# Performance work log

Measured on AMD Instinct MI355X. Metric: run time of the kernel, lower is better.

The kernel has to match this reference:

```python
import jax, jax.numpy as jnp
import numpy as np

H = 2048      # hidden_size
NH = 16       # num attention heads
KVH = 4       # num kv heads (GQA)
D = 128       # head_dim
E = 32        # num experts
K = 4         # top-k experts per token
I = 768       # moe intermediate size
T = 1024      # num tokens (single prefill sequence)
EPS = 1e-6
THETA = 10000.0


def rmsnorm(x, w, eps=EPS):
    return x * jax.lax.rsqrt(jnp.mean(x * x, axis=-1, keepdims=True) + eps) * w


def rope_cos_sin(positions, dim, theta):
    inv_freq = 1.0 / (theta ** (jnp.arange(0, dim, 2, dtype=jnp.float32) / dim))
    freqs = positions.astype(jnp.float32)[:, None] * inv_freq[None, :]   # [T, D/2]
    emb = jnp.concatenate([freqs, freqs], axis=-1)                       # [T, D]
    return jnp.cos(emb), jnp.sin(emb)


def apply_rope(x, cos, sin):
    # x: [T, nH, D]; cos/sin: [T, D] -> neox style: cat(-x2, x1)
    x1, x2 = jnp.split(x, 2, axis=-1)
    x_rot = jnp.concatenate([-x2, x1], axis=-1)
    return cos[:, None, :] * x + sin[:, None, :] * x_rot


def setup_inputs() -> dict:
    key = jax.random.key(0)
    ks = jax.random.split(key, 8)
    s = 0.02
    return {
        "hidden_states": jax.random.normal(ks[0], (T, H), jnp.float32),
        "positions": jnp.arange(T, dtype=jnp.int32),
        "ln1_w": jnp.ones((H,), jnp.float32),
        "w_qkv": jax.random.normal(ks[1], ((NH + 2 * KVH) * D, H), jnp.float32) * s,
        "q_norm_w": jnp.ones((D,), jnp.float32),
        "k_norm_w": jnp.ones((D,), jnp.float32),
        "w_o": jax.random.normal(ks[2], (H, NH * D), jnp.float32) * s,
        "ln2_w": jnp.ones((H,), jnp.float32),
        "router_w": jax.random.normal(ks[3], (E, H), jnp.float32) * s,
        "w_gate": jax.random.normal(ks[4], (E, I, H), jnp.float32) * s,
        "w_up": jax.random.normal(ks[5], (E, I, H), jnp.float32) * s,
        "w_down": jax.random.normal(ks[6], (E, H, I), jnp.float32) * s,
    }


def decoder_layer(hidden_states, positions, ln1_w, w_qkv, q_norm_w, k_norm_w,
                  w_o, ln2_w, router_w, w_gate, w_up, w_down):
    # ---- attention block ----
    residual = hidden_states
    h = rmsnorm(hidden_states, ln1_w)

    qkv = h @ w_qkv.T                                      # [T, (NH+2*KVH)*D]
    q, k, v = jnp.split(qkv, [NH * D, (NH + KVH) * D], axis=-1)
    q = q.reshape(T, NH, D)
    k = k.reshape(T, KVH, D)
    v = v.reshape(T, KVH, D)

    # per-head RMSNorm on q and k (Qwen3 QK-norm)
    q = rmsnorm(q, q_norm_w)
    k = rmsnorm(k, k_norm_w)

    cos, sin = rope_cos_sin(positions, D, THETA)
    q = apply_rope(q, cos, sin)
    k = apply_rope(k, cos, sin)

    rep = NH // KVH
    k = jnp.repeat(k, rep, axis=1)                         # [T, NH, D]
    v = jnp.repeat(v, rep, axis=1)

    scale = D ** -0.5
    scores = jnp.einsum("qhd,khd->hqk", q, k) * scale      # [NH, T, T]
    causal = jnp.tril(jnp.ones((T, T), bool))
    scores = jnp.where(causal[None], scores, -1e30)
    probs = jax.nn.softmax(scores, axis=-1)
    attn = jnp.einsum("hqk,khd->qhd", probs, v).reshape(T, NH * D)
    attn_out = attn @ w_o.T                                # [T, H]

    hidden = residual + attn_out

    # ---- MoE block ----
    residual = hidden
    h = rmsnorm(hidden, ln2_w)

    logits = h @ router_w.T                                # [T, E]
    router_probs = jax.nn.softmax(logits, axis=-1)
    topk_w, topk_idx = jax.lax.top_k(router_probs, K)      # softmax-then-topk
    topk_w = topk_w / (jnp.sum(topk_w, axis=-1, keepdims=True) + 1e-20)

    # scatter top-k weights into a dense [T, E] combine matrix
    combine = jnp.zeros((T, E), h.dtype).at[
        jnp.arange(T)[:, None], topk_idx].add(topk_w)

    gate = jnp.einsum("th,eih->tei", h, w_gate)            # [T, E, I]
    up = jnp.einsum("th,eih->tei", h, w_up)
    act = jax.nn.silu(gate) * up
    moe_out = jnp.einsum("tei,ehi,te->th", act, w_down, combine)

    return residual + moe_out


def reference(hidden_states, positions, ln1_w, w_qkv, q_norm_w, k_norm_w,
              w_o, ln2_w, router_w, w_gate, w_up, w_down):
    return decoder_layer(hidden_states, positions, ln1_w, w_qkv, q_norm_w,
                         k_norm_w, w_o, ln2_w, router_w, w_gate, w_up, w_down)
```

## Files before the change

### kernel.cpp

```cpp
#include <hip/hip_runtime.h>

typedef __attribute__((ext_vector_type(4))) float f32x4;
typedef __attribute__((ext_vector_type(8))) __bf16 bf16x8;
typedef __attribute__((ext_vector_type(4))) __bf16 bf16x4;

__device__ __forceinline__ f32x4 mfma16(bf16x8 a, bf16x8 b, f32x4 c) {
  return __builtin_amdgcn_mfma_f32_16x16x32_bf16(a, b, c, 0, 0, 0);
}

__global__ __launch_bounds__(256) void rmsnorm_k(const float* __restrict__ x,
                                                 const float* __restrict__ w,
                                                 float* __restrict__ y,
                                                 __bf16* __restrict__ yb) {
  int t = blockIdx.x;
  const float* xr = x + (size_t)t * 2048;
  int d0 = threadIdx.x * 4;
  float4 v1 = *(const float4*)(xr + d0);
  float4 v2 = *(const float4*)(xr + 1024 + d0);
  float ss = v1.x*v1.x + v1.y*v1.y + v1.z*v1.z + v1.w*v1.w
           + v2.x*v2.x + v2.y*v2.y + v2.z*v2.z + v2.w*v2.w;
#pragma unroll
  for (int mk = 1; mk < 64; mk <<= 1) ss += __shfl_xor(ss, mk);
  __shared__ float red[4];
  if ((threadIdx.x & 63) == 0) red[threadIdx.x >> 6] = ss;
  __syncthreads();
  float tot = red[0] + red[1] + red[2] + red[3];
  float rs = rsqrtf(tot * (1.0f / 2048.0f) + 1e-6f);
  float* yr = y + (size_t)t * 2048;
  float4 w1 = *(const float4*)(w + d0);
  float4 w2 = *(const float4*)(w + 1024 + d0);
  float4 o1, o2;
  o1.x = v1.x*rs*w1.x; o1.y = v1.y*rs*w1.y; o1.z = v1.z*rs*w1.z; o1.w = v1.w*rs*w1.w;
  o2.x = v2.x*rs*w2.x; o2.y = v2.y*rs*w2.y; o2.z = v2.z*rs*w2.z; o2.w = v2.w*rs*w2.w;
  *(float4*)(yr + d0) = o1;
  *(float4*)(yr + 1024 + d0) = o2;
  if (yb) {
    bf16x4 b1, b2;
    b1[0] = (__bf16)o1.x; b1[1] = (__bf16)o1.y; b1[2] = (__bf16)o1.z; b1[3] = (__bf16)o1.w;
    b2[0] = (__bf16)o2.x; b2[1] = (__bf16)o2.y; b2[2] = (__bf16)o2.z; b2[3] = (__bf16)o2.w;
    *(bf16x4*)(yb + (size_t)t * 2048 + d0) = b1;
    *(bf16x4*)(yb + (size_t)t * 2048 + 1024 + d0) = b2;
  }
}

__global__ __launch_bounds__(256) void gemm3_k(const float* __restrict__ A,
                                               const float* __restrict__ B,
                                               const float* __restrict__ RESID,
                                               float* __restrict__ C, int N, int K) {
  __shared__ __align__(16) __bf16 smAh[128 * 40];
  __shared__ __align__(16) __bf16 smAl[128 * 40];
  __shared__ __align__(16) __bf16 smBh[64 * 40];
  __shared__ __align__(16) __bf16 smBl[64 * 40];
  const int m0 = blockIdx.x * 128, n0 = blockIdx.y * 64;
  const int tid = threadIdx.x, l = tid & 63, w = tid >> 6;
  const int wm = w >> 1, wn = w & 1;
  float4 ra[4], rb[2];
#pragma unroll
  for (int i = 0; i < 4; i++) {
    int c = tid + i * 256, row = c >> 3, k4 = c & 7;
    ra[i] = *(const float4*)(A + (size_t)(m0 + row) * K + k4 * 4);
  }
#pragma unroll
  for (int i = 0; i < 2; i++) {
    int c = tid + i * 256, row = c >> 3, k4 = c & 7;
    rb[i] = *(const float4*)(B + (size_t)(n0 + row) * K + k4 * 4);
  }
  f32x4 acc[4][2] = {};
  for (int kt = 0; kt < K; kt += 32) {
    __syncthreads();
#pragma unroll
    for (int i = 0; i < 4; i++) {
      int c = tid + i * 256, row = c >> 3, k4 = c & 7;
      bf16x4 hv, lv;
#pragma unroll
      for (int j = 0; j < 4; j++) {
        float f = ((const float*)&ra[i])[j];
        __bf16 h = (__bf16)f; hv[j] = h; lv[j] = (__bf16)(f - (float)h);
      }
      *(bf16x4*)(smAh + row * 40 + k4 * 4) = hv;
      *(bf16x4*)(smAl + row * 40 + k4 * 4) = lv;
    }
#pragma unroll
    for (int i = 0; i < 2; i++) {
      int c = tid + i * 256, row = c >> 3, k4 = c & 7;
      bf16x4 hv, lv;
#pragma unroll
      for (int j = 0; j < 4; j++) {
        float f = ((const float*)&rb[i])[j];
        __bf16 h = (__bf16)f; hv[j] = h; lv[j] = (__bf16)(f - (float)h);
      }
      *(bf16x4*)(smBh + row * 40 + k4 * 4) = hv;
      *(bf16x4*)(smBl + row * 40 + k4 * 4) = lv;
    }
    __syncthreads();
    if (kt + 32 < K) {
#pragma unroll
      for (int i = 0; i < 4; i++) {
        int c = tid + i * 256, row = c >> 3, k4 = c & 7;
        ra[i] = *(const float4*)(A + (size_t)(m0 + row) * K + kt + 32 + k4 * 4);
      }
#pragma unroll
      for (int i = 0; i < 2; i++) {
        int c = tid + i * 256, row = c >> 3, k4 = c & 7;
        rb[i] = *(const float4*)(B + (size_t)(n0 + row) * K + kt + 32 + k4 * 4);
      }
    }
    bf16x8 ah[4], al[4], bh[2], bl[2];
    const int ko = (l >> 4) * 8;
#pragma unroll
    for (int f = 0; f < 4; f++) {
      int ar = wm * 64 + f * 16 + (l & 15);
      ah[f] = *(const bf16x8*)(smAh + ar * 40 + ko);
      al[f] = *(const bf16x8*)(smAl + ar * 40 + ko);
    }
#pragma unroll
    for (int f = 0; f < 2; f++) {
      int br = wn * 32 + f * 16 + (l & 15);
      bh[f] = *(const bf16x8*)(smBh + br * 40 + ko);
      bl[f] = *(const bf16x8*)(smBl + br * 40 + ko);
    }
#pragma unroll
    for (int mf = 0; mf < 4; mf++)
#pragma unroll
      for (int nf = 0; nf < 2; nf++) {
        acc[mf][nf] = mfma16(ah[mf], bh[nf], acc[mf][nf]);
        acc[mf][nf] = mfma16(ah[mf], bl[nf], acc[mf][nf]);
        acc[mf][nf] = mfma16(al[mf], bh[nf], acc[mf][nf]);
      }
  }
#pragma unroll
  for (int mf = 0; mf < 4; mf++) {
    int row = m0 + wm * 64 + mf * 16 + ((l >> 4) << 2);
#pragma unroll
    for (int nf = 0; nf < 2; nf++) {
      int col = n0 + wn * 32 + nf * 16 + (l & 15);
#pragma unroll
      for (int r = 0; r < 4; r++) {
        float v = acc[mf][nf][r];
        if (RESID) v += RESID[(size_t)(row + r) * N + col];
        C[(size_t)(row + r) * N + col] = v;
      }
    }
  }
}

__global__ __launch_bounds__(128) void qkr_k(const float* __restrict__ qkv,
                                             const int* __restrict__ pos,
                                             const float* __restrict__ qw,
                                             const float* __restrict__ kw,
                                             __bf16* __restrict__ qh, __bf16* __restrict__ ql,
                                             __bf16* __restrict__ kh, __bf16* __restrict__ kl,
                                             __bf16* __restrict__ vh, __bf16* __restrict__ vl) {
  int hs = blockIdx.x, t = blockIdx.y, d = threadIdx.x;
  float x = qkv[(size_t)t * 3072 + hs * 128 + d];
  __shared__ float xs[128];
  __shared__ float red[2];
  float o;
  if (hs < 20) {
    float ss = x * x;
#pragma unroll
    for (int mk = 1; mk < 64; mk <<= 1) ss += __shfl_xor(ss, mk);
    if ((d & 63) == 0) red[d >> 6] = ss;
    __syncthreads();
    float rs = rsqrtf((red[0] + red[1]) * (1.0f / 128.0f) + 1e-6f);
    const float* w = (hs < 16) ? qw : kw;
    float xn = x * rs * w[d];
    xs[d] = xn;
    __syncthreads();
    int i = d & 63;
    float invf = (float)pow(10000.0, -(double)i / 64.0);
    float ang = (float)pos[t] * invf;
    float cf = (float)cos((double)ang);
    float sf = (float)sin((double)ang);
    float rot = (d < 64) ? -xs[d + 64] : xs[d - 64];
    o = cf * xn + sf * rot;
  } else {
    o = x;
  }
  __bf16 hi = (__bf16)o;
  __bf16 lo = (__bf16)(o - (float)hi);
  if (hs < 16) {
    size_t idx = ((size_t)hs * 1024 + t) * 128 + d;
    qh[idx] = hi; ql[idx] = lo;
  } else if (hs < 20) {
    size_t idx = ((size_t)(hs - 16) * 1024 + t) * 128 + d;
    kh[idx] = hi; kl[idx] = lo;
  } else {
    size_t idx = ((size_t)(hs - 20) * 1024 + t) * 128 + d;
    vh[idx] = hi; vl[idx] = lo;
  }
}

__global__ void vtrans_k(const __bf16* __restrict__ vh, const __bf16* __restrict__ vl,
                         __bf16* __restrict__ vhT, __bf16* __restrict__ vlT) {
  __shared__ __bf16 tile[32][33];
  int kv = blockIdx.z, t0 = blockIdx.x * 32, d0 = blockIdx.y * 32;
  int tx = threadIdx.x, ty = threadIdx.y;
  tile[ty][tx] = vh[((size_t)kv * 1024 + t0 + ty) * 128 + d0 + tx];
  __syncthreads();
  vhT[((size_t)kv * 128 + d0 + ty) * 1024 + t0 + tx] = tile[tx][ty];
  __syncthreads();
  tile[ty][tx] = vl[((size_t)kv * 1024 + t0 + ty) * 128 + d0 + tx];
  __syncthreads();
  vlT[((size_t)kv * 128 + d0 + ty) * 1024 + t0 + tx] = tile[tx][ty];
}

__global__ __launch_bounds__(256) void flash_k(const __bf16* __restrict__ qh, const __bf16* __restrict__ ql,
                                               const __bf16* __restrict__ kh, const __bf16* __restrict__ kl,
                                               const __bf16* __restrict__ vhT, const __bf16* __restrict__ vlT,
                                               float* __restrict__ attn) {
  constexpr int KH = 0, KL = 4352, VH = 8704, VL = 13824, PH = 18944, PL = 21504;
  __shared__ __align__(16) __bf16 sm[24064];
  const int qt = blockIdx.x, h = blockIdx.y;
  const int q0 = qt * 64, kvh = h >> 2;
  const int tid = threadIdx.x, l = tid & 63, w = tid >> 6;
  for (int c = tid; c < 1024; c += 256) {
    int row = c >> 4, dc = c & 15;
    size_t g = ((size_t)h * 1024 + q0 + row) * 128 + dc * 8;
    *(bf16x8*)(sm + row * 136 + dc * 8) = *(const bf16x8*)(qh + g);
    *(bf16x8*)(sm + 8704 + row * 136 + dc * 8) = *(const bf16x8*)(ql + g);
  }
  __syncthreads();
  bf16x8 fqh[4], fql[4];
  {
    int row = w * 16 + (l & 15);
    int ko = (l >> 4) * 8;
#pragma unroll
    for (int kk = 0; kk < 4; kk++) {
      fqh[kk] = *(const bf16x8*)(sm + row * 136 + kk * 32 + ko);
      fql[kk] = *(const bf16x8*)(sm + 8704 + row * 136 + kk * 32 + ko);
    }
  }
  f32x4 acc[8] = {};
  float m_run[4], l_run[4];
#pragma unroll
  for (int r = 0; r < 4; r++) { m_run[r] = -1e30f; l_run[r] = 0.0f; }
  const int ktiles = (q0 + 64) >> 5;
  for (int kt = 0; kt < ktiles; kt++) {
    const int k0 = kt * 32;
    __syncthreads();
    for (int c = tid; c < 512; c += 256) {
      int row = c >> 4, dc = c & 15;
      size_t g = ((size_t)kvh * 1024 + k0 + row) * 128 + dc * 8;
      *(bf16x8*)(sm + KH + row * 136 + dc * 8) = *(const bf16x8*)(kh + g);
      *(bf16x8*)(sm + KL + row * 136 + dc * 8) = *(const bf16x8*)(kl + g);
    }
    for (int c = tid; c < 512; c += 256) {
      int row = c >> 2, tc = c & 3;
      size_t g = ((size_t)kvh * 128 + row) * 1024 + k0 + tc * 8;
      *(bf16x8*)(sm + VH + row * 40 + tc * 8) = *(const bf16x8*)(vhT + g);
      *(bf16x8*)(sm + VL + row * 40 + tc * 8) = *(const bf16x8*)(vlT + g);
    }
    __syncthreads();
    f32x4 s[2] = {};
#pragma unroll
    for (int kk = 0; kk < 4; kk++) {
      int ko = kk * 32 + (l >> 4) * 8;
#pragma unroll
      for (int nf = 0; nf < 2; nf++) {
        int key = nf * 16 + (l & 15);
        bf16x8 bh_ = *(const bf16x8*)(sm + KH + key * 136 + ko);
        bf16x8 bl_ = *(const bf16x8*)(sm + KL + key * 136 + ko);
        s[nf] = mfma16(fqh[kk], bh_, s[nf]);
        s[nf] = mfma16(fqh[kk], bl_, s[nf]);
        s[nf] = mfma16(fql[kk], bh_, s[nf]);
      }
    }
    const float scale = 0.08838834764831845f;
    const bool need_mask = (k0 + 31 > q0);
    float p[2][4], alpha[4];
#pragma unroll
    for (int r = 0; r < 4; r++) {
      float s0 = s[0][r] * scale, s1 = s[1][r] * scale;
      if (need_mask) {
        int qi = q0 + w * 16 + ((l >> 4) << 2) + r;
        if (k0 + (l & 15) > qi) s0 = -1e30f;
        if (k0 + 16 + (l & 15) > qi) s1 = -1e30f;
      }
      float mt = fmaxf(s0, s1);
#pragma unroll
      for (int mk = 1; mk < 16; mk <<= 1) mt = fmaxf(mt, __shfl_xor(mt, mk));
      float mnew = fmaxf(m_run[r], mt);
      alpha[r] = expf(m_run[r] - mnew);
      float p0 = expf(s0 - mnew), p1 = expf(s1 - mnew);
      float rs = p0 + p1;
#pragma unroll
      for (int mk = 1; mk < 16; mk <<= 1) rs += __shfl_xor(rs, mk);
      l_run[r] = l_run[r] * alpha[r] + rs;
      m_run[r] = mnew;
      p[0][r] = p0; p[1][r] = p1;
    }
#pragma unroll
    for (int nf2 = 0; nf2 < 8; nf2++)
#pragma unroll
      for (int r = 0; r < 4; r++) acc[nf2][r] *= alpha[r];
    const int phb = PH + w * 640, plb = PL + w * 640;
#pragma unroll
    for (int nf = 0; nf < 2; nf++)
#pragma unroll
      for (int r = 0; r < 4; r++) {
        int row = ((l >> 4) << 2) + r, col = nf * 16 + (l & 15);
        __bf16 hi = (__bf16)p[nf][r];
        sm[phb + row * 40 + col] = hi;
        sm[plb + row * 40 + col] = (__bf16)(p[nf][r] - (float)hi);
      }
    bf16x8 aph = *(const bf16x8*)(sm + phb + (l & 15) * 40 + (l >> 4) * 8);
    bf16x8 apl = *(const bf16x8*)(sm + plb + (l & 15) * 40 + (l >> 4) * 8);
#pragma unroll
    for (int nf2 = 0; nf2 < 8; nf2++) {
      int drow = nf2 * 16 + (l & 15);
      bf16x8 bvh = *(const bf16x8*)(sm + VH + drow * 40 + (l >> 4) * 8);
      bf16x8 bvl = *(const bf16x8*)(sm + VL + drow * 40 + (l >> 4) * 8);
      acc[nf2] = mfma16(aph, bvh, acc[nf2]);
      acc[nf2] = mfma16(aph, bvl, acc[nf2]);
      acc[nf2] = mfma16(apl, bvh, acc[nf2]);
    }
  }
#pragma unroll
  for (int r = 0; r < 4; r++) {
    float inv = 1.0f / l_run[r];
    size_t t = q0 + w * 16 + ((l >> 4) << 2) + r;
#pragma unroll
    for (int nf2 = 0; nf2 < 8; nf2++)
      attn[t * 2048 + h * 128 + nf2 * 16 + (l & 15)] = acc[nf2][r] * inv;
  }
}

__global__ __launch_bounds__(256) void router_k(const float* __restrict__ h2,
                                                const float* __restrict__ rw,
                                                int* __restrict__ tidx, float* __restrict__ tw,
                                                int* __restrict__ counts) {
  int t = blockIdx.x;
  int e = threadIdx.x >> 3, sub = threadIdx.x & 7;
  const float* hrow = h2 + (size_t)t * 2048;
  const float* wrow = rw + (size_t)e * 2048;
  float acc = 0.0f;
  for (int d = sub * 4; d < 2048; d += 32) {
    float4 a = *(const float4*)(hrow + d);
    float4 b = *(const float4*)(wrow + d);
    acc += a.x * b.x + a.y * b.y + a.z * b.z + a.w * b.w;
  }
  acc += __shfl_xor(acc, 1); acc += __shfl_xor(acc, 2); acc += __shfl_xor(acc, 4);
  __shared__ float lg[32];
  if (sub == 0) lg[e] = acc;
  __syncthreads();
  if (threadIdx.x < 64) {
    int l = threadIdx.x;
    float v = (l < 32) ? lg[l] : -3e38f;
    float mx = v;
#pragma unroll
    for (int mk = 1; mk < 32; mk <<= 1) mx = fmaxf(mx, __shfl_xor(mx, mk));
    float ex = (l < 32) ? expf(v - mx) : 0.0f;
    float den = ex;
#pragma unroll
    for (int mk = 1; mk < 32; mk <<= 1) den += __shfl_xor(den, mk);
    float prob = ex / den;
    float pv = v;
    int sel_i[4]; float sel_w[4]; float wsum = 0.0f;
#pragma unroll
    for (int j = 0; j < 4; j++) {
      float m2 = pv;
#pragma unroll
      for (int mk = 1; mk < 32; mk <<= 1) m2 = fmaxf(m2, __shfl_xor(m2, mk));
      unsigned long long ball = __ballot((pv == m2) && (l < 32));
      int sel = __ffsll(ball) - 1;
      float ps = __shfl(prob, sel);
      sel_i[j] = sel; sel_w[j] = ps; wsum += ps;
      if (l == sel) pv = -3e38f;
    }
    if (l < 4) {
      tidx[t * 4 + l] = sel_i[l];
      tw[t * 4 + l] = sel_w[l] / (wsum + 1e-20f);
      atomicAdd(&counts[sel_i[l]], 1);
    }
  }
}

__global__ void zero_k(int* counts) { if (threadIdx.x < 32) counts[threadIdx.x] = 0; }

__global__ void scan_k(const int* __restrict__ counts, int* __restrict__ offs,
                       int* __restrict__ cursor, int* __restrict__ pair_e,
                       int* __restrict__ pair_mt) {
  int l = threadIdx.x;
  int c = (l < 32) ? counts[l] : 0;
  int x = c;
#pragma unroll
  for (int d = 1; d < 32; d <<= 1) {
    int y = __shfl_up(x, d);
    if (l >= d) x += y;
  }
  if (l < 32) { offs[l] = x - c; cursor[l] = 0; }
  if (l == 31) offs[32] = x;
  if (l == 0) {
    int n = 0;
    for (int e = 0; e < 32; e++) {
      int ce = counts[e];
      for (int m = 0; m * 128 < ce; m++) { pair_e[n] = e; pair_mt[n] = m; n++; }
    }
    for (; n < 64; n++) { pair_e[n] = -1; pair_mt[n] = 0; }
  }
}

__global__ __launch_bounds__(256) void scatter_k(const int* __restrict__ tidx,
                                                 const int* __restrict__ offs,
                                                 int* __restrict__ cursor,
                                                 int* __restrict__ row_of_slot,
                                                 int* __restrict__ tok_of_row) {
  int p = blockIdx.x * 256 + threadIdx.x;
  if (p >= 4096) return;
  int e = tidx[p];
  int pos = atomicAdd(&cursor[e], 1);
  int row = offs[e] + pos;
  row_of_slot[p] = row;
  tok_of_row[row] = p >> 2;
}

__global__ __launch_bounds__(256) void gateup_k(const __bf16* __restrict__ h2b,
                                                const float* __restrict__ wg,
                                                const float* __restrict__ wu,
                                                const int* __restrict__ counts,
                                                const int* __restrict__ offs,
                                                const int* __restrict__ tok_of_row,
                                                const int* __restrict__ pair_e,
                                                const int* __restrict__ pair_mt,
                                                float* __restrict__ gu) {
  const int p = blockIdx.y;
  const int e = pair_e[p];
  if (e < 0) return;
  const int mt = pair_mt[p];
  const int cnt = counts[e];
  const int j = blockIdx.x;
  const float* wsel = (j < 12) ? wg : wu;
  const int n0 = (j < 12 ? j : j - 12) * 64;
  const int gout = (j < 12) ? 0 : 768;
  __shared__ __align__(16) __bf16 smA[128 * 40];
  __shared__ __align__(16) __bf16 smB[64 * 40];
  __shared__ int toks[128];
  const int tid = threadIdx.x, l = tid & 63, w = tid >> 6;
  const int wm = w >> 1, wn = w & 1;
  if (tid < 128) {
    int r = mt * 128 + tid;
    toks[tid] = (r < cnt) ? tok_of_row[offs[e] + r] : tok_of_row[offs[e]];
  }
  __syncthreads();
  const float* we = wsel + (size_t)e * 768 * 2048;
  bf16x8 ra[2]; float4 rb[2];
#pragma unroll
  for (int i = 0; i < 2; i++) {
    int c = tid + i * 256, row = c >> 2, kc = c & 3;
    ra[i] = *(const bf16x8*)(h2b + (size_t)toks[row] * 2048 + kc * 8);
  }
#pragma unroll
  for (int i = 0; i < 2; i++) {
    int c = tid + i * 256, row = c >> 3, k4 = c & 7;
    rb[i] = *(const float4*)(we + (size_t)(n0 + row) * 2048 + k4 * 4);
  }
  f32x4 acc[4][2] = {};
  for (int kt = 0; kt < 2048; kt += 32) {
    __syncthreads();
#pragma unroll
    for (int i = 0; i < 2; i++) {
      int c = tid + i * 256, row = c >> 2, kc = c & 3;
      *(bf16x8*)(smA + row * 40 + kc * 8) = ra[i];
    }
#pragma unroll
    for (int i = 0; i < 2; i++) {
      int c = tid + i * 256, row = c >> 3, k4 = c & 7;
      bf16x4 hv;
#pragma unroll
      for (int q = 0; q < 4; q++) hv[q] = (__bf16)((const float*)&rb[i])[q];
      *(bf16x4*)(smB + row * 40 + k4 * 4) = hv;
    }
    __syncthreads();
    if (kt + 32 < 2048) {
#pragma unroll
      for (int i = 0; i < 2; i++) {
        int c = tid + i * 256, row = c >> 2, kc = c & 3;
        ra[i] = *(const bf16x8*)(h2b + (size_t)toks[row] * 2048 + kt + 32 + kc * 8);
      }
#pragma unroll
      for (int i = 0; i < 2; i++) {
        int c = tid + i * 256, row = c >> 3, k4 = c & 7;
        rb[i] = *(const float4*)(we + (size_t)(n0 + row) * 2048 + kt + 32 + k4 * 4);
      }
    }
    bf16x8 af[4], bf_[2];
    const int ko = (l >> 4) * 8;
#pragma unroll
    for (int f = 0; f < 4; f++)
      af[f] = *(const bf16x8*)(smA + (wm * 64 + f * 16 + (l & 15)) * 40 + ko);
#pragma unroll
    for (int f = 0; f < 2; f++)
      bf_[f] = *(const bf16x8*)(smB + (wn * 32 + f * 16 + (l & 15)) * 40 + ko);
#pragma unroll
    for (int mf = 0; mf < 4; mf++)
#pragma unroll
      for (int nf = 0; nf < 2; nf++)
        acc[mf][nf] = mfma16(af[mf], bf_[nf], acc[mf][nf]);
  }
#pragma unroll
  for (int mf = 0; mf < 4; mf++) {
    int rr = mt * 128 + wm * 64 + mf * 16 + ((l >> 4) << 2);
#pragma unroll
    for (int nf = 0; nf < 2; nf++) {
      int col = gout + n0 + wn * 32 + nf * 16 + (l & 15);
#pragma unroll
      for (int r = 0; r < 4; r++)
        if (rr + r < cnt)
          gu[(size_t)(offs[e] + rr + r) * 1536 + col] = acc[mf][nf][r];
    }
  }
}

__global__ __launch_bounds__(192) void silu_k(const float* __restrict__ gu,
                                              __bf16* __restrict__ act) {
  int r = blockIdx.x, c = threadIdx.x * 4;
  float4 g = *(const float4*)(gu + (size_t)r * 1536 + c);
  float4 u = *(const float4*)(gu + (size_t)r * 1536 + 768 + c);
  bf16x4 o;
  o[0] = (__bf16)(g.x / (1.0f + expf(-g.x)) * u.x);
  o[1] = (__bf16)(g.y / (1.0f + expf(-g.y)) * u.y);
  o[2] = (__bf16)(g.z / (1.0f + expf(-g.z)) * u.z);
  o[3] = (__bf16)(g.w / (1.0f + expf(-g.w)) * u.w);
  *(bf16x4*)(act + (size_t)r * 768 + c) = o;
}

__global__ __launch_bounds__(256) void down_k(const __bf16* __restrict__ act,
                                              const float* __restrict__ wd,
                                              const int* __restrict__ counts,
                                              const int* __restrict__ offs,
                                              const int* __restrict__ pair_e,
                                              const int* __restrict__ pair_mt,
                                              float* __restrict__ dout) {
  const int p = blockIdx.y;
  const int e = pair_e[p];
  if (e < 0) return;
  const int mt = pair_mt[p];
  const int cnt = counts[e];
  const int n0 = blockIdx.x * 64;
  __shared__ __align__(16) __bf16 smA[128 * 40];
  __shared__ __align__(16) __bf16 smB[64 * 40];
  const int tid = threadIdx.x, l = tid & 63, w = tid >> 6;
  const int wm = w >> 1, wn = w & 1;
  const float* wde = wd + (size_t)e * 2048 * 768;
  const int base = offs[e] + mt * 128;
  bf16x8 ra[2]; float4 rb[2];
#pragma unroll
  for (int i = 0; i < 2; i++) {
    int c = tid + i * 256, row = c >> 2, kc = c & 3;
    int rg = base + row; if (rg > 4095) rg = 4095;
    ra[i] = *(const bf16x8*)(act + (size_t)rg * 768 + kc * 8);
  }
#pragma unroll
  for (int i = 0; i < 2; i++) {
    int c = tid + i * 256, row = c >> 3, k4 = c & 7;
    rb[i] = *(const float4*)(wde + (size_t)(n0 + row) * 768 + k4 * 4);
  }
  f32x4 acc[4][2] = {};
  for (int kt = 0; kt < 768; kt += 32) {
    __syncthreads();
#pragma unroll
    for (int i = 0; i < 2; i++) {
      int c = tid + i * 256, row = c >> 2, kc = c & 3;
      *(bf16x8*)(smA + row * 40 + kc * 8) = ra[i];
    }
#pragma unroll
    for (int i = 0; i < 2; i++) {
      int c = tid + i * 256, row = c >> 3, k4 = c & 7;
      bf16x4 hv;
#pragma unroll
      for (int q = 0; q < 4; q++) hv[q] = (__bf16)((const float*)&rb[i])[q];
      *(bf16x4*)(smB + row * 40 + k4 * 4) = hv;
    }
    __syncthreads();
    if (kt + 32 < 768) {
#pragma unroll
      for (int i = 0; i < 2; i++) {
        int c = tid + i * 256, row = c >> 2, kc = c & 3;
        int rg = base + row; if (rg > 4095) rg = 4095;
        ra[i] = *(const bf16x8*)(act + (size_t)rg * 768 + kt + 32 + kc * 8);
      }
#pragma unroll
      for (int i = 0; i < 2; i++) {
        int c = tid + i * 256, row = c >> 3, k4 = c & 7;
        rb[i] = *(const float4*)(wde + (size_t)(n0 + row) * 768 + kt + 32 + k4 * 4);
      }
    }
    bf16x8 af[4], bf_[2];
    const int ko = (l >> 4) * 8;
#pragma unroll
    for (int f = 0; f < 4; f++)
      af[f] = *(const bf16x8*)(smA + (wm * 64 + f * 16 + (l & 15)) * 40 + ko);
#pragma unroll
    for (int f = 0; f < 2; f++)
      bf_[f] = *(const bf16x8*)(smB + (wn * 32 + f * 16 + (l & 15)) * 40 + ko);
#pragma unroll
    for (int mf = 0; mf < 4; mf++)
#pragma unroll
      for (int nf = 0; nf < 2; nf++)
        acc[mf][nf] = mfma16(af[mf], bf_[nf], acc[mf][nf]);
  }
#pragma unroll
  for (int mf = 0; mf < 4; mf++) {
    int rr = mt * 128 + wm * 64 + mf * 16 + ((l >> 4) << 2);
#pragma unroll
    for (int nf = 0; nf < 2; nf++) {
      int col = n0 + wn * 32 + nf * 16 + (l & 15);
#pragma unroll
      for (int r = 0; r < 4; r++)
        if (rr + r < cnt)
          dout[(size_t)(offs[e] + rr + r) * 2048 + col] = acc[mf][nf][r];
    }
  }
}

__global__ __launch_bounds__(256) void combine_k(const float* __restrict__ hidden,
                                                 const float* __restrict__ dout,
                                                 const int* __restrict__ row_of_slot,
                                                 const float* __restrict__ tw,
                                                 float* __restrict__ out) {
  int t = blockIdx.x;
  int r0 = row_of_slot[t * 4 + 0], r1 = row_of_slot[t * 4 + 1];
  int r2 = row_of_slot[t * 4 + 2], r3 = row_of_slot[t * 4 + 3];
  float w0 = tw[t * 4 + 0], w1 = tw[t * 4 + 1], w2 = tw[t * 4 + 2], w3 = tw[t * 4 + 3];
  const float* h = hidden + (size_t)t * 2048;
  float* o = out + (size_t)t * 2048;
  for (int d = threadIdx.x * 4; d < 2048; d += 1024) {
    float4 hv = *(const float4*)(h + d);
    float4 a0 = *(const float4*)(dout + (size_t)r0 * 2048 + d);
    float4 a1 = *(const float4*)(dout + (size_t)r1 * 2048 + d);
    float4 a2 = *(const float4*)(dout + (size_t)r2 * 2048 + d);
    float4 a3 = *(const float4*)(dout + (size_t)r3 * 2048 + d);
    float4 ov;
    ov.x = hv.x + w0 * a0.x + w1 * a1.x + w2 * a2.x + w3 * a3.x;
    ov.y = hv.y + w0 * a0.y + w1 * a1.y + w2 * a2.y + w3 * a3.y;
    ov.z = hv.z + w0 * a0.z + w1 * a1.z + w2 * a2.z + w3 * a3.z;
    ov.w = hv.w + w0 * a0.w + w1 * a1.w + w2 * a2.w + w3 * a3.w;
    *(float4*)(o + d) = ov;
  }
}

extern "C" void kernel_launch(void* const* d_in, const int* in_sizes, int n_in,
                              void* d_out, int out_size, void* d_ws, size_t ws_size,
                              hipStream_t stream) {
  (void)in_sizes; (void)n_in; (void)out_size; (void)ws_size;
  const float* hs   = (const float*)d_in[0];
  const int*   pos  = (const int*)d_in[1];
  const float* ln1w = (const float*)d_in[2];
  const float* wqkv = (const float*)d_in[3];
  const float* qnw  = (const float*)d_in[4];
  const float* knw  = (const float*)d_in[5];
  const float* wo   = (const float*)d_in[6];
  const float* ln2w = (const float*)d_in[7];
  const float* rw   = (const float*)d_in[8];
  const float* wg   = (const float*)d_in[9];
  const float* wu   = (const float*)d_in[10];
  const float* wd   = (const float*)d_in[11];
  float* out = (float*)d_out;
  char* ws = (char*)d_ws;

  float*  h1     = (float*)(ws + 0);
  float*  gu     = (float*)(ws + 0);
  float*  dout   = (float*)(ws + 0);
  float*  qkv    = (float*)(ws + 8388608);
  __bf16* qh     = (__bf16*)(ws + 20971520);
  __bf16* ql     = (__bf16*)(ws + 25165824);
  __bf16* kh     = (__bf16*)(ws + 29360128);
  __bf16* kl     = (__bf16*)(ws + 30408704);
  __bf16* vh     = (__bf16*)(ws + 31457280);
  __bf16* vl     = (__bf16*)(ws + 32505856);
  __bf16* vhT    = (__bf16*)(ws + 33554432);
  __bf16* vlT    = (__bf16*)(ws + 34603008);
  int*    pair_e = (int*)(ws + 33554432);
  int*    pair_mt= (int*)(ws + 33554944);
  float*  attn   = (float*)(ws + 35651584);
  __bf16* h2b    = (__bf16*)(ws + 35651584);
  __bf16* act    = (__bf16*)(ws + 35651584);
  float*  hidden = (float*)(ws + 44040192);
  float*  h2     = (float*)(ws + 52428800);
  int*    tidx   = (int*)(ws + 60817408);
  float*  tw     = (float*)(ws + 60833792);
  int*    counts = (int*)(ws + 60850176);
  int*    offs   = (int*)(ws + 60850432);
  int*    cursor = (int*)(ws + 60850688);
  int*    row_of_slot = (int*)(ws + 60850944);
  int*    tok_of_row  = (int*)(ws + 60867328);

  rmsnorm_k<<<1024, 256, 0, stream>>>(hs, ln1w, h1, nullptr);
  gemm3_k<<<dim3(8, 48), 256, 0, stream>>>(h1, wqkv, nullptr, qkv, 3072, 2048);
  qkr_k<<<dim3(24, 1024), 128, 0, stream>>>(qkv, pos, qnw, knw, qh, ql, kh, kl, vh, vl);
  vtrans_k<<<dim3(32, 4, 4), dim3(32, 32), 0, stream>>>(vh, vl, vhT, vlT);
  flash_k<<<dim3(16, 16), 256, 0, stream>>>(qh, ql, kh, kl, vhT, vlT, attn);
  gemm3_k<<<dim3(8, 32), 256, 0, stream>>>(attn, wo, hs, hidden, 2048, 2048);

  rmsnorm_k<<<1024, 256, 0, stream>>>(hidden, ln2w, h2, h2b);
  zero_k<<<1, 64, 0, stream>>>(counts);
  router_k<<<1024, 256, 0, stream>>>(h2, rw, tidx, tw, counts);
  scan_k<<<1, 64, 0, stream>>>(counts, offs, cursor, pair_e, pair_mt);
  scatter_k<<<16, 256, 0, stream>>>(tidx, offs, cursor, row_of_slot, tok_of_row);
  gateup_k<<<dim3(24, 64), 256, 0, stream>>>(h2b, wg, wu, counts, offs, tok_of_row, pair_e, pair_mt, gu);
  silu_k<<<4096, 192, 0, stream>>>(gu, act);
  down_k<<<dim3(32, 64), 256, 0, stream>>>(act, wd, counts, offs, pair_e, pair_mt, dout);
  combine_k<<<1024, 256, 0, stream>>>(hidden, dout, row_of_slot, tw, out);
}
```

Baseline: 610.0 us.

## Load MoE A fragments directly to registers and double-buffer weight tiles

In the MoE gate/up and down GEMMs, the activation (A) operand no longer goes through shared memory. Each lane loads its MFMA fragment straight from global memory, using per-row pointers computed once. The weight (B) tile becomes double-buffered in LDS, with two k-steps of 32 per loop iteration and prefetch registers running further ahead, which halves the barriers per k-step. This is meant to cut LDS traffic and synchronisation and to overlap global loads with MFMA work, in exchange for more registers and uncoalesced per-lane A loads.

```diff
diff --git a/kernel.cpp b/kernel.cpp
--- a/kernel.cpp
+++ b/kernel.cpp
@@ -433,8 +433,7 @@
   const float* wsel = (j < 12) ? wg : wu;
   const int n0 = (j < 12 ? j : j - 12) * 64;
   const int gout = (j < 12) ? 0 : 768;
-  __shared__ __align__(16) __bf16 smA[128 * 40];
-  __shared__ __align__(16) __bf16 smB[64 * 40];
+  __shared__ __align__(16) __bf16 smB[2][64 * 40];
   __shared__ int toks[128];
   const int tid = threadIdx.x, l = tid & 63, w = tid >> 6;
   const int wm = w >> 1, wn = w & 1;
@@ -443,60 +442,99 @@
     toks[tid] = (r < cnt) ? tok_of_row[offs[e] + r] : tok_of_row[offs[e]];
   }
   __syncthreads();
+  const int ko = (l >> 4) * 8;
+  const __bf16* aptr[4];
+#pragma unroll
+  for (int f = 0; f < 4; f++)
+    aptr[f] = h2b + (size_t)toks[wm * 64 + f * 16 + (l & 15)] * 2048 + ko;
   const float* we = wsel + (size_t)e * 768 * 2048;
-  bf16x8 ra[2]; float4 rb[2];
+  const float* bptr[2];
 #pragma unroll
   for (int i = 0; i < 2; i++) {
-    int c = tid + i * 256, row = c >> 2, kc = c & 3;
-    ra[i] = *(const bf16x8*)(h2b + (size_t)toks[row] * 2048 + kc * 8);
-  }
-#pragma unroll
-  for (int i = 0; i < 2; i++) {
-    int c = tid + i * 256, row = c >> 3, k4 = c & 7;
-    rb[i] = *(const float4*)(we + (size_t)(n0 + row) * 2048 + k4 * 4);
-  }
+    int c = tid + i * 256;
+    bptr[i] = we + (size_t)(n0 + (c >> 3)) * 2048 + (c & 7) * 4;
+  }
+  const int bo0 = (tid >> 3) * 40 + (tid & 7) * 4;
+  const int bo1 = ((tid + 256) >> 3) * 40 + (tid & 7) * 4;
+  const int bf0 = (wn * 32 + (l & 15)) * 40 + ko;
+  const int bf1 = (wn * 32 + 16 + (l & 15)) * 40 + ko;
+
+  float4 rbE0, rbE1, rbO0, rbO1;
+  bf16x8 aA[4], aB[4];
+  rbE0 = *(const float4*)(bptr[0]);      rbE1 = *(const float4*)(bptr[1]);
+  rbO0 = *(const float4*)(bptr[0] + 32); rbO1 = *(const float4*)(bptr[1] + 32);
+#pragma unroll
+  for (int f = 0; f < 4; f++) { aA[f] = *(const bf16x8*)(aptr[f]); aB[f] = *(const bf16x8*)(aptr[f] + 32); }
+  {
+    bf16x4 hv;
+#pragma unroll
+    for (int q = 0; q < 4; q++) hv[q] = (__bf16)((const float*)&rbE0)[q];
+    *(bf16x4*)(&smB[0][0] + bo0) = hv;
+#pragma unroll
+    for (int q = 0; q < 4; q++) hv[q] = (__bf16)((const float*)&rbE1)[q];
+    *(bf16x4*)(&smB[0][0] + bo1) = hv;
+  }
+  rbE0 = *(const float4*)(bptr[0] + 64); rbE1 = *(const float4*)(bptr[1] + 64);
+  __syncthreads();
+
   f32x4 acc[4][2] = {};
-  for (int kt = 0; kt < 2048; kt += 32) {
-    __syncthreads();
-#pragma unroll
-    for (int i = 0; i < 2; i++) {
-      int c = tid + i * 256, row = c >> 2, kc = c & 3;
-      *(bf16x8*)(smA + row * 40 + kc * 8) = ra[i];
-    }
-#pragma unroll
-    for (int i = 0; i < 2; i++) {
-      int c = tid + i * 256, row = c >> 3, k4 = c & 7;
+  for (int kt = 0; kt < 2048; kt += 64) {
+    {
       bf16x4 hv;
 #pragma unroll
-      for (int q = 0; q < 4; q++) hv[q] = (__bf16)((const float*)&rb[i])[q];
-      *(bf16x4*)(smB + row * 40 + k4 * 4) = hv;
-    }
-    __syncthreads();
-    if (kt + 32 < 2048) {
-#pragma unroll
-      for (int i = 0; i < 2; i++) {
-        int c = tid + i * 256, row = c >> 2, kc = c & 3;
-        ra[i] = *(const bf16x8*)(h2b + (size_t)toks[row] * 2048 + kt + 32 + kc * 8);
-      }
-#pragma unroll
-      for (int i = 0; i < 2; i++) {
-        int c = tid + i * 256, row = c >> 3, k4 = c & 7;
-        rb[i] = *(const float4*)(we + (size_t)(n0 + row) * 2048 + kt + 32 + k4 * 4);
-      }
-    }
-    bf16x8 af[4], bf_[2];
-    const int ko = (l >> 4) * 8;
-#pragma unroll
-    for (int f = 0; f < 4; f++)
-      af[f] = *(const bf16x8*)(smA + (wm * 64 + f * 16 + (l & 15)) * 40 + ko);
-#pragma unroll
-    for (int f = 0; f < 2; f++)
-      bf_[f] = *(const bf16x8*)(smB + (wn * 32 + f * 16 + (l & 15)) * 40 + ko);
-#pragma unroll
-    for (int mf = 0; mf < 4; mf++)
-#pragma unroll
-      for (int nf = 0; nf < 2; nf++)
-        acc[mf][nf] = mfma16(af[mf], bf_[nf], acc[mf][nf]);
+      for (int q = 0; q < 4; q++) hv[q] = (__bf16)((const float*)&rbO0)[q];
+      *(bf16x4*)(&smB[1][0] + bo0) = hv;
+#pragma unroll
+      for (int q = 0; q < 4; q++) hv[q] = (__bf16)((const float*)&rbO1)[q];
+      *(bf16x4*)(&smB[1][0] + bo1) = hv;
+    }
+    {
+      int kn = (kt + 96 < 2048) ? kt + 96 : 0;
+      rbO0 = *(const float4*)(bptr[0] + kn); rbO1 = *(const float4*)(bptr[1] + kn);
+    }
+    {
+      bf16x8 b0 = *(const bf16x8*)(&smB[0][0] + bf0);
+      bf16x8 b1 = *(const bf16x8*)(&smB[0][0] + bf1);
+#pragma unroll
+      for (int mf = 0; mf < 4; mf++) {
+        acc[mf][0] = mfma16(aA[mf], b0, acc[mf][0]);
+        acc[mf][1] = mfma16(aA[mf], b1, acc[mf][1]);
+      }
+    }
+    {
+      int ka = (kt + 64 < 2048) ? kt + 64 : 0;
+#pragma unroll
+      for (int f = 0; f < 4; f++) aA[f] = *(const bf16x8*)(aptr[f] + ka);
+    }
+    __syncthreads();
+    {
+      bf16x4 hv;
+#pragma unroll
+      for (int q = 0; q < 4; q++) hv[q] = (__bf16)((const float*)&rbE0)[q];
+      *(bf16x4*)(&smB[0][0] + bo0) = hv;
+#pragma unroll
+      for (int q = 0; q < 4; q++) hv[q] = (__bf16)((const float*)&rbE1)[q];
+      *(bf16x4*)(&smB[0][0] + bo1) = hv;
+    }
+    {
+      int kn = (kt + 128 < 2048) ? kt + 128 : 0;
+      rbE0 = *(const float4*)(bptr[0] + kn); rbE1 = *(const float4*)(bptr[1] + kn);
+    }
+    {
+      bf16x8 b0 = *(const bf16x8*)(&smB[1][0] + bf0);
+      bf16x8 b1 = *(const bf16x8*)(&smB[1][0] + bf1);
+#pragma unroll
+      for (int mf = 0; mf < 4; mf++) {
+        acc[mf][0] = mfma16(aB[mf], b0, acc[mf][0]);
+        acc[mf][1] = mfma16(aB[mf], b1, acc[mf][1]);
+      }
+    }
+    {
+      int ka = (kt + 96 < 2048) ? kt + 96 : 0;
+#pragma unroll
+      for (int f = 0; f < 4; f++) aB[f] = *(const bf16x8*)(aptr[f] + ka);
+    }
+    __syncthreads();
   }
 #pragma unroll
   for (int mf = 0; mf < 4; mf++) {
@@ -538,67 +576,106 @@
   const int mt = pair_mt[p];
   const int cnt = counts[e];
   const int n0 = blockIdx.x * 64;
-  __shared__ __align__(16) __bf16 smA[128 * 40];
-  __shared__ __align__(16) __bf16 smB[64 * 40];
+  __shared__ __align__(16) __bf16 smB[2][64 * 40];
   const int tid = threadIdx.x, l = tid & 63, w = tid >> 6;
   const int wm = w >> 1, wn = w & 1;
   const float* wde = wd + (size_t)e * 2048 * 768;
   const int base = offs[e] + mt * 128;
-  bf16x8 ra[2]; float4 rb[2];
+  const int ko = (l >> 4) * 8;
+  const __bf16* aptr[4];
+#pragma unroll
+  for (int f = 0; f < 4; f++) {
+    int rg = base + wm * 64 + f * 16 + (l & 15);
+    if (rg > 4095) rg = 4095;
+    aptr[f] = act + (size_t)rg * 768 + ko;
+  }
+  const float* bptr[2];
 #pragma unroll
   for (int i = 0; i < 2; i++) {
-    int c = tid + i * 256, row = c >> 2, kc = c & 3;
-    int rg = base + row; if (rg > 4095) rg = 4095;
-    ra[i] = *(const bf16x8*)(act + (size_t)rg * 768 + kc * 8);
-  }
-#pragma unroll
-  for (int i = 0; i < 2; i++) {
-    int c = tid + i * 256, row = c >> 3, k4 = c & 7;
-    rb[i] = *(const float4*)(wde + (size_t)(n0 + row) * 768 + k4 * 4);
-  }
+    int c = tid + i * 256;
+    bptr[i] = wde + (size_t)(n0 + (c >> 3)) * 768 + (c & 7) * 4;
+  }
+  const int bo0 = (tid >> 3) * 40 + (tid & 7) * 4;
+  const int bo1 = ((tid + 256) >> 3) * 40 + (tid & 7) * 4;
+  const int bf0 = (wn * 32 + (l & 15)) * 40 + ko;
+  const int bf1 = (wn * 32 + 16 + (l & 15)) * 40 + ko;
+
+  float4 rbE0, rbE1, rbO0, rbO1;
+  bf16x8 aA[4], aB[4];
+  rbE0 = *(const float4*)(bptr[0]);      rbE1 = *(const float4*)(bptr[1]);
+  rbO0 = *(const float4*)(bptr[0] + 32); rbO1 = *(const float4*)(bptr[1] + 32);
+#pragma unroll
+  for (int f = 0; f < 4; f++) { aA[f] = *(const bf16x8*)(aptr[f]); aB[f] = *(const bf16x8*)(aptr[f] + 32); }
+  {
+    bf16x4 hv;
+#pragma unroll
+    for (int q = 0; q < 4; q++) hv[q] = (__bf16)((const float*)&rbE0)[q];
+    *(bf16x4*)(&smB[0][0] + bo0) = hv;
+#pragma unroll
+    for (int q = 0; q < 4; q++) hv[q] = (__bf16)((const float*)&rbE1)[q];
+    *(bf16x4*)(&smB[0][0] + bo1) = hv;
+  }
+  rbE0 = *(const float4*)(bptr[0] + 64); rbE1 = *(const float4*)(bptr[1] + 64);
+  __syncthreads();
+
   f32x4 acc[4][2] = {};
-  for (int kt = 0; kt < 768; kt += 32) {
-    __syncthreads();
-#pragma unroll
-    for (int i = 0; i < 2; i++) {
-      int c = tid + i * 256, row = c >> 2, kc = c & 3;
-      *(bf16x8*)(smA + row * 40 + kc * 8) = ra[i];
-    }
-#pragma unroll
-    for (int i = 0; i < 2; i++) {
-      int c = tid + i * 256, row = c >> 3, k4 = c & 7;
+  for (int kt = 0; kt < 768; kt += 64) {
+    {
       bf16x4 hv;
 #pragma unroll
-      for (int q = 0; q < 4; q++) hv[q] = (__bf16)((const float*)&rb[i])[q];
-      *(bf16x4*)(smB + row * 40 + k4 * 4) = hv;
-    }
-    __syncthreads();
-    if (kt + 32 < 768) {
-#pragma unroll
-      for (int i = 0; i < 2; i++) {
-        int c = tid + i * 256, row = c >> 2, kc = c & 3;
-        int rg = base + row; if (rg > 4095) rg = 4095;
-        ra[i] = *(const bf16x8*)(act + (size_t)rg * 768 + kt + 32 + kc * 8);
-      }
-#pragma unroll
-      for (int i = 0; i < 2; i++) {
-        int c = tid + i * 256, row = c >> 3, k4 = c & 7;
-        rb[i] = *(const float4*)(wde + (size_t)(n0 + row) * 768 + kt + 32 + k4 * 4);
-      }
-    }
-    bf16x8 af[4], bf_[2];
-    const int ko = (l >> 4) * 8;
-#pragma unroll
-    for (int f = 0; f < 4; f++)
-      af[f] = *(const bf16x8*)(smA + (wm * 64 + f * 16 + (l & 15)) * 40 + ko);
-#pragma unroll
-    for (int f = 0; f < 2; f++)
-      bf_[f] = *(const bf16x8*)(smB + (wn * 32 + f * 16 + (l & 15)) * 40 + ko);
-#pragma unroll
-    for (int mf = 0; mf < 4; mf++)
-#pragma unroll
-      for (int nf = 0; nf < 2; nf++)
-        acc[mf][nf] = mfma16(af[mf], bf_[nf], acc[mf][nf]);
+      for (int q = 0; q < 4; q++) hv[q] = (__bf16)((const float*)&rbO0)[q];
+      *(bf16x4*)(&smB[1][0] + bo0) = hv;
+#pragma unroll
+      for (int q = 0; q < 4; q++) hv[q] = (__bf16)((const float*)&rbO1)[q];
+      *(bf16x4*)(&smB[1][0] + bo1) = hv;
+    }
+    {
+      int kn = (kt + 96 < 768) ? kt + 96 : 0;
+      rbO0 = *(const float4*)(bptr[0] + kn); rbO1 = *(const float4*)(bptr[1] + kn);
+    }
+    {
+      bf16x8 b0 = *(const bf16x8*)(&smB[0][0] + bf0);
+      bf16x8 b1 = *(const bf16x8*)(&smB[0][0] + bf1);
+#pragma unroll
+      for (int mf = 0; mf < 4; mf++) {
+        acc[mf][0] = mfma16(aA[mf], b0, acc[mf][0]);
+        acc[mf][1] = mfma16(aA[mf], b1, acc[mf][1]);
+      }
+    }
+    {
+      int ka = (kt + 64 < 768) ? kt + 64 : 0;
+#pragma unroll
+      for (int f = 0; f < 4; f++) aA[f] = *(const bf16x8*)(aptr[f] + ka);
+    }
+    __syncthreads();
+    {
+      bf16x4 hv;
+#pragma unroll
+      for (int q = 0; q < 4; q++) hv[q] = (__bf16)((const float*)&rbE0)[q];
+      *(bf16x4*)(&smB[0][0] + bo0) = hv;
+#pragma unroll
+      for (int q = 0; q < 4; q++) hv[q] = (__bf16)((const float*)&rbE1)[q];
+      *(bf16x4*)(&smB[0][0] + bo1) = hv;
+    }
+    {
+      int kn = (kt + 128 < 768) ? kt + 128 : 0;
+      rbE0 = *(const float4*)(bptr[0] + kn); rbE1 = *(const float4*)(bptr[1] + kn);
+    }
+    {
+      bf16x8 b0 = *(const bf16x8*)(&smB[1][0] + bf0);
+      bf16x8 b1 = *(const bf16x8*)(&smB[1][0] + bf1);
+#pragma unroll
+      for (int mf = 0; mf < 4; mf++) {
+        acc[mf][0] = mfma16(aB[mf], b0, acc[mf][0]);
+        acc[mf][1] = mfma16(aB[mf], b1, acc[mf][1]);
+      }
+    }
+    {
+      int ka = (kt + 96 < 768) ? kt + 96 : 0;
+#pragma unroll
+      for (int f = 0; f < 4; f++) aB[f] = *(const bf16x8*)(aptr[f] + ka);
+    }
+    __syncthreads();
   }
 #pragma unroll
   for (int mf = 0; mf < 4; mf++) {
```

New measurement: 668.2 us. +9.5%, slower.
